# Optimization experiments

Measured on AMD Instinct MI355X. Metric: run time of the kernel, lower is better.

The kernel has to match this reference:

```python
import jax, jax.numpy as jnp
import numpy as np

EPS = 1e-5

def _bn_bcn(x, g, b):
    # BatchNorm1d on [B, C, N], training mode: stats over (B, N) per channel
    m = x.mean(axis=(0, 2), keepdims=True)
    v = x.var(axis=(0, 2), keepdims=True)
    return g[None, :, None] * (x - m) * jax.lax.rsqrt(v + EPS) + b[None, :, None]

def _bn_bc(x, g, b):
    # BatchNorm1d on [B, C]
    m = x.mean(axis=0)
    v = x.var(axis=0)
    return g * (x - m) * jax.lax.rsqrt(v + EPS) + b

def _symmetric_orthogonalization(x9):
    # x9: [B, 9] -> [B, 3, 3] in SO(3)
    m = x9.reshape(-1, 3, 3)
    u, s, vt = jnp.linalg.svd(m, full_matrices=False)
    det = jnp.linalg.det(jnp.matmul(u, vt))[:, None, None]
    vt = jnp.concatenate([vt[:, :2, :], vt[:, 2:, :] * det], axis=1)
    return jnp.matmul(u, vt)

def setup_inputs() -> dict:
    key = jax.random.key(0)
    ks = jax.random.split(key, 24)
    B, N = 32, 2048
    def lin(k, out_c, in_c):
        return jax.random.normal(k, (out_c, in_c), jnp.float32) / np.sqrt(in_c)
    inp = {}
    inp['x'] = jax.random.normal(ks[0], (B, 3, N), jnp.float32)
    # conv1x1 weights (kernel size 1 -> per-point linear)
    inp['w1'] = lin(ks[1], 64, 3);    inp['b1'] = jnp.zeros((64,), jnp.float32)
    inp['g1'] = jnp.ones((64,), jnp.float32);   inp['be1'] = jnp.zeros((64,), jnp.float32)
    inp['w2'] = lin(ks[2], 128, 64);  inp['b2'] = jnp.zeros((128,), jnp.float32)
    inp['g2'] = jnp.ones((128,), jnp.float32);  inp['be2'] = jnp.zeros((128,), jnp.float32)
    inp['w3'] = lin(ks[3], 1024, 128); inp['b3'] = jnp.zeros((1024,), jnp.float32)
    inp['g3'] = jnp.ones((1024,), jnp.float32); inp['be3'] = jnp.zeros((1024,), jnp.float32)
    inp['wf1'] = lin(ks[4], 512, 1024); inp['bf1'] = jnp.zeros((512,), jnp.float32)
    inp['gf1'] = jnp.ones((512,), jnp.float32); inp['bef1'] = jnp.zeros((512,), jnp.float32)
    inp['wf2'] = lin(ks[5], 256, 512);  inp['bf2'] = jnp.zeros((256,), jnp.float32)
    inp['gf2'] = jnp.ones((256,), jnp.float32); inp['bef2'] = jnp.zeros((256,), jnp.float32)
    inp['wp'] = lin(ks[6], 12, 256);    inp['bp'] = jnp.zeros((12,), jnp.float32)
    return inp

def reference(x, w1, b1, g1, be1, w2, b2, g2, be2, w3, b3, g3, be3,
              wf1, bf1, gf1, bef1, wf2, bf2, gf2, bef2, wp, bp):
    B = x.shape[0]
    h = jax.nn.relu(_bn_bcn(jnp.einsum('bdn,od->bon', x, w1) + b1[None, :, None], g1, be1))
    h = jax.nn.relu(_bn_bcn(jnp.einsum('bdn,od->bon', h, w2) + b2[None, :, None], g2, be2))
    h = _bn_bcn(jnp.einsum('bdn,od->bon', h, w3) + b3[None, :, None], g3, be3)
    h = jnp.max(h, axis=2)                      # global max pool -> [B, 1024]
    h = jax.nn.relu(_bn_bc(h @ wf1.T + bf1, gf1, bef1))
    h = jax.nn.relu(_bn_bc(h @ wf2.T + bf2, gf2, bef2))
    p = h @ wp.T + bp                           # [B, 12]
    R = _symmetric_orthogonalization(p[:, :9])  # [B, 3, 3]
    t = p[:, 9:].reshape(-1, 3, 1)
    top = jnp.concatenate([R, t], axis=2)       # [B, 3, 4]
    pad = jnp.broadcast_to(jnp.array([0.0, 0.0, 0.0, 1.0], dtype=x.dtype), (B, 1, 4))
    return jnp.concatenate([top, pad], axis=1)  # [B, 4, 4]
```

## Files before the change

kernel.cpp:

```cpp
#include <hip/hip_runtime.h>


#define NPT 2048
#define C1 64
#define C2 128
#define EPSV 1e-5f

typedef __attribute__((ext_vector_type(8))) _Float16 half8;
typedef __attribute__((ext_vector_type(4))) float floatx4;

#define OFF_Y1H   0
#define OFF_Y2H   2097152
#define OFF_Z     6291456
#define OFF_SUM1  (OFF_Z)
#define OFF_SQ1   (OFF_Z+64)
#define OFF_SUM2  (OFF_Z+128)
#define OFF_SQ2   (OFF_Z+256)
#define OFF_SUM3  (OFF_Z+384)
#define OFF_SQ3   (OFF_Z+1408)
#define OFF_F1R   (OFF_Z+2432)
#define OFF_F2R   (OFF_Z+18816)
#define ZN        27008
#define OFF_MX    (OFF_Z+27008)
#define OFF_MN    (OFF_MX+131072)
#define OFF_POOL  (OFF_MN+131072)
#define OFF_W3H   (OFF_POOL+32768)
#define OFF_W2H   (OFF_W3H+65536)
#define WS_FLOATS (OFF_W2H+4096)

static __device__ inline unsigned short f16r(float f) {
  _Float16 h = (_Float16)f;
  return __builtin_bit_cast(unsigned short, h);
}
static __device__ inline float h2f(unsigned short u) {
  return (float)__builtin_bit_cast(_Float16, u);
}
static __device__ inline int SW(int n, int cb) { return n ^ (((n >> 3) ^ cb) & 7); }

__global__ __launch_bounds__(256) void k_conv1(const float* __restrict__ x,
    const float* __restrict__ w1, const float* __restrict__ b1,
    unsigned short* __restrict__ y1h, float* __restrict__ sum1, float* __restrict__ sq1)
{
  int idx4 = blockIdx.x * 256 + threadIdx.x;
  int n4 = idx4 & 511;
  int o  = (idx4 >> 9) & 63;
  int b  = idx4 >> 15;
  const float4* xr = (const float4*)(x + (size_t)b * 3 * NPT);
  float4 x0 = xr[n4], x1 = xr[512 + n4], x2 = xr[1024 + n4];
  float wa = w1[o*3], wb = w1[o*3+1], wc = w1[o*3+2], bb = b1[o];
  float4 v;
  v.x = fmaf(wa, x0.x, fmaf(wb, x1.x, fmaf(wc, x2.x, bb)));
  v.y = fmaf(wa, x0.y, fmaf(wb, x1.y, fmaf(wc, x2.y, bb)));
  v.z = fmaf(wa, x0.z, fmaf(wb, x1.z, fmaf(wc, x2.z, bb)));
  v.w = fmaf(wa, x0.w, fmaf(wb, x1.w, fmaf(wc, x2.w, bb)));
  ushort4 p;
  p.x = f16r(v.x); p.y = f16r(v.y); p.z = f16r(v.z); p.w = f16r(v.w);
  ((ushort4*)y1h)[idx4] = p;
  float s = v.x + v.y + v.z + v.w;
  float q = v.x*v.x + v.y*v.y + v.z*v.z + v.w*v.w;
  for (int off = 32; off; off >>= 1) { s += __shfl_down(s, off); q += __shfl_down(q, off); }
  __shared__ float red[8];
  int lane = threadIdx.x & 63, wv = threadIdx.x >> 6;
  if (!lane) { red[wv] = s; red[4 + wv] = q; }
  __syncthreads();
  if (!threadIdx.x) {
    atomicAdd(&sum1[o], red[0] + red[1] + red[2] + red[3]);
    atomicAdd(&sq1[o],  red[4] + red[5] + red[6] + red[7]);
  }
}

__global__ __launch_bounds__(256) void k_cvt(const float* __restrict__ w3,
    const float* __restrict__ w2, unsigned short* __restrict__ w3h,
    unsigned short* __restrict__ w2h)
{
  int idx4 = blockIdx.x * 256 + threadIdx.x;
  const float4* src; ushort4* dst; int k;
  if (idx4 < 32768) { src = (const float4*)w3; dst = (ushort4*)w3h; k = idx4; }
  else               { src = (const float4*)w2; dst = (ushort4*)w2h; k = idx4 - 32768; }
  float4 v = src[k];
  ushort4 o;
  o.x = f16r(v.x); o.y = f16r(v.y); o.z = f16r(v.z); o.w = f16r(v.w);
  dst[k] = o;
}

__global__ __launch_bounds__(256, 2) void k_conv2(const unsigned short* __restrict__ y1h,
    const unsigned short* __restrict__ w2h, const float* __restrict__ b2,
    const float* __restrict__ sum1, const float* __restrict__ sq1,
    const float* __restrict__ g1, const float* __restrict__ be1,
    unsigned short* __restrict__ y2h, float* __restrict__ sum2, float* __restrict__ sq2)
{
  __shared__ unsigned short w2s[8 * 128 * 8];
  __shared__ unsigned short h1s[8 * 64 * 8];
  __shared__ float bn1[64][2];
  __shared__ float sred[2][128][2];
  int t = threadIdx.x;
  int bi = blockIdx.x;
  int b = bi >> 5, ns = bi & 31;
  int n0 = ns * 64;
  int w = t >> 6, lane = t & 63;
  int ow = w & 1, nw = w >> 1;
  int quad = lane >> 4, l15 = lane & 15;

  if (t < 64) {
    float m = sum1[t] * (1.f / 65536.f);
    float v = fmaf(-m, m, sq1[t] * (1.f / 65536.f));
    float ia = g1[t] * rsqrtf(v + EPSV);
    bn1[t][0] = ia; bn1[t][1] = fmaf(-ia, m, be1[t]);
  }
  for (int i = 0; i < 4; ++i) {
    int idx = i * 256 + t;
    int o = idx >> 3, cb = idx & 7;
    uint4 v = *(const uint4*)(w2h + o * 64 + cb * 8);
    int op = (o + cb) & 127;
    *(uint4*)&w2s[(cb * 128 + op) * 8] = v;
  }
  __syncthreads();

  half8 af[4][2];
  #pragma unroll
  for (int ti = 0; ti < 4; ++ti)
    #pragma unroll
    for (int s = 0; s < 2; ++s) {
      int cb = s * 4 + quad;
      int o = ow * 64 + ti * 16 + l15;
      int op = (o + cb) & 127;
      af[ti][s] = *(const half8*)&w2s[(cb * 128 + op) * 8];
    }
  float breg[4][4];
  #pragma unroll
  for (int ti = 0; ti < 4; ++ti)
    #pragma unroll
    for (int r = 0; r < 4; ++r)
      breg[ti][r] = b2[ow * 64 + ti * 16 + quad * 4 + r];

  {
    int cg = t >> 5, ng = t & 31;
    int c0 = cg * 8, nn = ng * 2;
    float av[8], sv[8];
    #pragma unroll
    for (int i = 0; i < 8; ++i) { av[i] = bn1[c0 + i][0]; sv[i] = bn1[c0 + i][1]; }
    const unsigned short* yb = y1h + (size_t)(b * C1 + c0) * NPT + n0 + nn;
    float v0[8], v1[8];
    #pragma unroll
    for (int i = 0; i < 8; ++i) {
      unsigned u = *(const unsigned*)(yb + (size_t)i * NPT);
      v0[i] = fmaxf(fmaf(av[i], h2f((unsigned short)(u & 0xffffu)), sv[i]), 0.f);
      v1[i] = fmaxf(fmaf(av[i], h2f((unsigned short)(u >> 16)), sv[i]), 0.f);
    }
    uint4 pk;
    pk.x = (unsigned)f16r(v0[0]) | ((unsigned)f16r(v0[1]) << 16);
    pk.y = (unsigned)f16r(v0[2]) | ((unsigned)f16r(v0[3]) << 16);
    pk.z = (unsigned)f16r(v0[4]) | ((unsigned)f16r(v0[5]) << 16);
    pk.w = (unsigned)f16r(v0[6]) | ((unsigned)f16r(v0[7]) << 16);
    *(uint4*)&h1s[(cg * 64 + SW(nn, cg)) * 8] = pk;
    pk.x = (unsigned)f16r(v1[0]) | ((unsigned)f16r(v1[1]) << 16);
    pk.y = (unsigned)f16r(v1[2]) | ((unsigned)f16r(v1[3]) << 16);
    pk.z = (unsigned)f16r(v1[4]) | ((unsigned)f16r(v1[5]) << 16);
    pk.w = (unsigned)f16r(v1[6]) | ((unsigned)f16r(v1[7]) << 16);
    *(uint4*)&h1s[(cg * 64 + SW(nn + 1, cg)) * 8] = pk;
  }
  __syncthreads();

  floatx4 acc[4][2];
  #pragma unroll
  for (int ti = 0; ti < 4; ++ti)
    #pragma unroll
    for (int nt = 0; nt < 2; ++nt) acc[ti][nt] = (floatx4){0.f, 0.f, 0.f, 0.f};
  #pragma unroll
  for (int s = 0; s < 2; ++s) {
    int cb = s * 4 + quad;
    half8 bf[2];
    #pragma unroll
    for (int nt = 0; nt < 2; ++nt) {
      int n = nw * 32 + nt * 16 + l15;
      bf[nt] = *(const half8*)&h1s[(cb * 64 + SW(n, cb)) * 8];
    }
    #pragma unroll
    for (int ti = 0; ti < 4; ++ti) {
      acc[ti][0] = __builtin_amdgcn_mfma_f32_16x16x32_f16(af[ti][s], bf[0], acc[ti][0], 0, 0, 0);
      acc[ti][1] = __builtin_amdgcn_mfma_f32_16x16x32_f16(af[ti][s], bf[1], acc[ti][1], 0, 0, 0);
    }
  }

  float sm[4][4], sq[4][4];
  #pragma unroll
  for (int ti = 0; ti < 4; ++ti)
    #pragma unroll
    for (int r = 0; r < 4; ++r) { sm[ti][r] = 0.f; sq[ti][r] = 0.f; }
  #pragma unroll
  for (int ti = 0; ti < 4; ++ti) {
    int o = ow * 64 + ti * 16 + quad * 4;
    #pragma unroll
    for (int nt = 0; nt < 2; ++nt) {
      int n = n0 + nw * 32 + nt * 16 + l15;
      #pragma unroll
      for (int r = 0; r < 4; ++r) {
        float val = acc[ti][nt][r] + breg[ti][r];
        y2h[(size_t)(b * C2 + o + r) * NPT + n] = f16r(val);
        sm[ti][r] += val;
        sq[ti][r] = fmaf(val, val, sq[ti][r]);
      }
    }
  }
  #pragma unroll
  for (int ti = 0; ti < 4; ++ti)
    #pragma unroll
    for (int r = 0; r < 4; ++r) {
      #pragma unroll
      for (int m = 1; m < 16; m <<= 1) {
        sm[ti][r] += __shfl_xor(sm[ti][r], m, 16);
        sq[ti][r] += __shfl_xor(sq[ti][r], m, 16);
      }
    }
  if (l15 == 0) {
    #pragma unroll
    for (int ti = 0; ti < 4; ++ti)
      #pragma unroll
      for (int r = 0; r < 4; ++r) {
        int oloc = ow * 64 + ti * 16 + quad * 4 + r;
        sred[nw][oloc][0] = sm[ti][r];
        sred[nw][oloc][1] = sq[ti][r];
      }
  }
  __syncthreads();
  if (t < 128) {
    atomicAdd(&sum2[t], sred[0][t][0] + sred[1][t][0]);
    atomicAdd(&sq2[t],  sred[0][t][1] + sred[1][t][1]);
  }
}

__global__ __launch_bounds__(256, 2) void k_conv3(const unsigned short* __restrict__ y2h,
    const unsigned short* __restrict__ w3h, const float* __restrict__ b3,
    const float* __restrict__ sum2, const float* __restrict__ sq2,
    const float* __restrict__ g2, const float* __restrict__ be2,
    float* __restrict__ mxb, float* __restrict__ mnb,
    float* __restrict__ sum3, float* __restrict__ sq3)
{
  __shared__ unsigned short w3s[16 * 128 * 8];
  __shared__ unsigned short h2s[16 * 64 * 8];
  __shared__ float sred[2][128][4];
  __shared__ float bn2[128][2];
  int t = threadIdx.x;
  int bi = blockIdx.x;
  int ot_blk = bi >> 7;
  int b  = (bi >> 2) & 31;
  int ns = bi & 3;
  int o0 = ot_blk * 128;
  int n_base = ns * 512;
  int w = t >> 6, lane = t & 63;
  int ow = w & 1, nw = w >> 1;
  int quad = lane >> 4, l15 = lane & 15;

  if (t < 128) {
    float m = sum2[t] * (1.f / 65536.f);
    float v = fmaf(-m, m, sq2[t] * (1.f / 65536.f));
    float ia = g2[t] * rsqrtf(v + EPSV);
    bn2[t][0] = ia; bn2[t][1] = fmaf(-ia, m, be2[t]);
  }
  for (int i = 0; i < 8; ++i) {
    int idx = i * 256 + t;
    int o = idx >> 4, cb = idx & 15;
    uint4 v = *(const uint4*)(w3h + (size_t)(o0 + o) * 128 + cb * 8);
    int op = (o + cb) & 127;
    *(uint4*)&w3s[(cb * 128 + op) * 8] = v;
  }
  __syncthreads();

  half8 af[4][4];
  #pragma unroll
  for (int ti = 0; ti < 4; ++ti)
    #pragma unroll
    for (int s = 0; s < 4; ++s) {
      int cb = s * 4 + quad;
      int o = ow * 64 + ti * 16 + l15;
      int op = (o + cb) & 127;
      af[ti][s] = *(const half8*)&w3s[(cb * 128 + op) * 8];
    }

  float breg[4][4], mx[4][4], mn[4][4], sm[4][4], sq[4][4];
  #pragma unroll
  for (int ti = 0; ti < 4; ++ti)
    #pragma unroll
    for (int r = 0; r < 4; ++r) {
      breg[ti][r] = b3[o0 + ow * 64 + ti * 16 + quad * 4 + r];
      mx[ti][r] = -3.4e38f; mn[ti][r] = 3.4e38f; sm[ti][r] = 0.f; sq[ti][r] = 0.f;
    }

  int cg = t >> 4, ng = t & 15;
  int c0 = cg * 8, nn = ng * 4;
  float av[8], sv[8];
  #pragma unroll
  for (int i = 0; i < 8; ++i) { av[i] = bn2[c0 + i][0]; sv[i] = bn2[c0 + i][1]; }

  for (int nc = 0; nc < 8; ++nc) {
    int n0 = n_base + nc * 64;
    __syncthreads();
    {
      float4 m[8];
      const unsigned short* yb = y2h + (size_t)(b * C2 + c0) * NPT + n0 + nn;
      #pragma unroll
      for (int i = 0; i < 8; ++i) {
        ushort4 u = *(const ushort4*)(yb + (size_t)i * NPT);
        m[i].x = fmaxf(fmaf(av[i], h2f(u.x), sv[i]), 0.f);
        m[i].y = fmaxf(fmaf(av[i], h2f(u.y), sv[i]), 0.f);
        m[i].z = fmaxf(fmaf(av[i], h2f(u.z), sv[i]), 0.f);
        m[i].w = fmaxf(fmaf(av[i], h2f(u.w), sv[i]), 0.f);
      }
      #define ST_J(j, comp) { \
        uint4 pk; \
        pk.x = (unsigned)f16r(m[0].comp) | ((unsigned)f16r(m[1].comp) << 16); \
        pk.y = (unsigned)f16r(m[2].comp) | ((unsigned)f16r(m[3].comp) << 16); \
        pk.z = (unsigned)f16r(m[4].comp) | ((unsigned)f16r(m[5].comp) << 16); \
        pk.w = (unsigned)f16r(m[6].comp) | ((unsigned)f16r(m[7].comp) << 16); \
        *(uint4*)&h2s[(cg * 64 + SW(nn + j, cg)) * 8] = pk; }
      ST_J(0, x) ST_J(1, y) ST_J(2, z) ST_J(3, w)
      #undef ST_J
    }
    __syncthreads();

    floatx4 acc[4][2];
    #pragma unroll
    for (int ti = 0; ti < 4; ++ti)
      #pragma unroll
      for (int nt = 0; nt < 2; ++nt) acc[ti][nt] = (floatx4){0.f, 0.f, 0.f, 0.f};
    #pragma unroll
    for (int s = 0; s < 4; ++s) {
      int cb = s * 4 + quad;
      half8 bf[2];
      #pragma unroll
      for (int nt = 0; nt < 2; ++nt) {
        int n = nw * 32 + nt * 16 + l15;
        bf[nt] = *(const half8*)&h2s[(cb * 64 + SW(n, cb)) * 8];
      }
      #pragma unroll
      for (int ti = 0; ti < 4; ++ti) {
        acc[ti][0] = __builtin_amdgcn_mfma_f32_16x16x32_f16(af[ti][s], bf[0], acc[ti][0], 0, 0, 0);
        acc[ti][1] = __builtin_amdgcn_mfma_f32_16x16x32_f16(af[ti][s], bf[1], acc[ti][1], 0, 0, 0);
      }
    }
    #pragma unroll
    for (int ti = 0; ti < 4; ++ti)
      #pragma unroll
      for (int nt = 0; nt < 2; ++nt)
        #pragma unroll
        for (int r = 0; r < 4; ++r) {
          float v = acc[ti][nt][r] + breg[ti][r];
          mx[ti][r] = fmaxf(mx[ti][r], v);
          mn[ti][r] = fminf(mn[ti][r], v);
          sm[ti][r] += v;
          sq[ti][r] = fmaf(v, v, sq[ti][r]);
        }
  }

  #pragma unroll
  for (int ti = 0; ti < 4; ++ti)
    #pragma unroll
    for (int r = 0; r < 4; ++r) {
      #pragma unroll
      for (int m = 1; m < 16; m <<= 1) {
        mx[ti][r] = fmaxf(mx[ti][r], __shfl_xor(mx[ti][r], m, 16));
        mn[ti][r] = fminf(mn[ti][r], __shfl_xor(mn[ti][r], m, 16));
        sm[ti][r] += __shfl_xor(sm[ti][r], m, 16);
        sq[ti][r] += __shfl_xor(sq[ti][r], m, 16);
      }
    }
  if (l15 == 0) {
    #pragma unroll
    for (int ti = 0; ti < 4; ++ti)
      #pragma unroll
      for (int r = 0; r < 4; ++r) {
        int oloc = ow * 64 + ti * 16 + quad * 4 + r;
        sred[nw][oloc][0] = mx[ti][r];
        sred[nw][oloc][1] = mn[ti][r];
        sred[nw][oloc][2] = sm[ti][r];
        sred[nw][oloc][3] = sq[ti][r];
      }
  }
  __syncthreads();
  if (t < 128) {
    int o = o0 + t;
    mxb[ns * 32768 + b * 1024 + o] = fmaxf(sred[0][t][0], sred[1][t][0]);
    mnb[ns * 32768 + b * 1024 + o] = fminf(sred[0][t][1], sred[1][t][1]);
    atomicAdd(&sum3[o], sred[0][t][2] + sred[1][t][2]);
    atomicAdd(&sq3[o],  sred[0][t][3] + sred[1][t][3]);
  }
}

__global__ __launch_bounds__(256) void k_pooled(const float* __restrict__ sum3,
    const float* __restrict__ sq3, const float* __restrict__ g3,
    const float* __restrict__ be3, const float* __restrict__ mxb,
    const float* __restrict__ mnb, float* __restrict__ pool)
{
  int idx4 = blockIdx.x * 256 + threadIdx.x;
  int c4 = idx4 & 255;
  float4 S = ((const float4*)sum3)[c4];
  float4 Q = ((const float4*)sq3)[c4];
  float4 G = ((const float4*)g3)[c4];
  float4 Be = ((const float4*)be3)[c4];
  float4 a, s;
  const float inv = 1.f / 65536.f;
  #define MK(c) { float m = S.c * inv; float v = fmaf(-m, m, Q.c * inv); \
                  a.c = G.c * rsqrtf(v + EPSV); s.c = fmaf(-a.c, m, Be.c); }
  MK(x) MK(y) MK(z) MK(w)
  #undef MK
  float4 mx = ((const float4*)mxb)[idx4];
  float4 mn = ((const float4*)mnb)[idx4];
  #pragma unroll
  for (int sl = 1; sl < 4; ++sl) {
    float4 mxs = ((const float4*)mxb)[idx4 + sl * 8192];
    float4 mns = ((const float4*)mnb)[idx4 + sl * 8192];
    mx.x = fmaxf(mx.x, mxs.x); mx.y = fmaxf(mx.y, mxs.y);
    mx.z = fmaxf(mx.z, mxs.z); mx.w = fmaxf(mx.w, mxs.w);
    mn.x = fminf(mn.x, mns.x); mn.y = fminf(mn.y, mns.y);
    mn.z = fminf(mn.z, mns.z); mn.w = fminf(mn.w, mns.w);
  }
  float4 r;
  r.x = fmaf(a.x, (a.x >= 0.f ? mx.x : mn.x), s.x);
  r.y = fmaf(a.y, (a.y >= 0.f ? mx.y : mn.y), s.y);
  r.z = fmaf(a.z, (a.z >= 0.f ? mx.z : mn.z), s.z);
  r.w = fmaf(a.w, (a.w >= 0.f ? mx.w : mn.w), s.w);
  ((float4*)pool)[idx4] = r;
}

__global__ __launch_bounds__(256) void k_fc1(const float* __restrict__ pool,
    const float* __restrict__ wf1, const float* __restrict__ bf1,
    float* __restrict__ f1r)
{
  __shared__ float ins[32 * 128];
  int t = threadIdx.x;
  int f0 = blockIdx.x * 32;
  int k0 = blockIdx.y * 128;
  #pragma unroll
  for (int i = 0; i < 4; ++i) {
    int idx = i * 256 + t;
    int b = idx >> 5, k4 = idx & 31;
    *(float4*)&ins[b * 128 + k4 * 4] = *(const float4*)(pool + (size_t)b * 1024 + k0 + k4 * 4);
  }
  __syncthreads();
  int f = t & 31, bq = t >> 5;
  int bl = bq * 4;
  const float4* wr = (const float4*)(wf1 + (size_t)(f0 + f) * 1024 + k0);
  float acc0 = 0.f, acc1 = 0.f, acc2 = 0.f, acc3 = 0.f;
  #pragma unroll
  for (int k4 = 0; k4 < 32; ++k4) {
    float4 wv = wr[k4];
    float4 i0 = *(const float4*)&ins[(bl + 0) * 128 + k4 * 4];
    float4 i1 = *(const float4*)&ins[(bl + 1) * 128 + k4 * 4];
    float4 i2 = *(const float4*)&ins[(bl + 2) * 128 + k4 * 4];
    float4 i3 = *(const float4*)&ins[(bl + 3) * 128 + k4 * 4];
    acc0 = fmaf(wv.x, i0.x, fmaf(wv.y, i0.y, fmaf(wv.z, i0.z, fmaf(wv.w, i0.w, acc0))));
    acc1 = fmaf(wv.x, i1.x, fmaf(wv.y, i1.y, fmaf(wv.z, i1.z, fmaf(wv.w, i1.w, acc1))));
    acc2 = fmaf(wv.x, i2.x, fmaf(wv.y, i2.y, fmaf(wv.z, i2.z, fmaf(wv.w, i2.w, acc2))));
    acc3 = fmaf(wv.x, i3.x, fmaf(wv.y, i3.y, fmaf(wv.z, i3.z, fmaf(wv.w, i3.w, acc3))));
  }
  float bs = (blockIdx.y == 0) ? bf1[f0 + f] : 0.f;
  atomicAdd(&f1r[(size_t)(bl + 0) * 512 + f0 + f], acc0 + bs);
  atomicAdd(&f1r[(size_t)(bl + 1) * 512 + f0 + f], acc1 + bs);
  atomicAdd(&f1r[(size_t)(bl + 2) * 512 + f0 + f], acc2 + bs);
  atomicAdd(&f1r[(size_t)(bl + 3) * 512 + f0 + f], acc3 + bs);
}

__global__ __launch_bounds__(256) void k_fc2(const float* __restrict__ f1r,
    const float* __restrict__ wf2, const float* __restrict__ bf2,
    const float* __restrict__ gf1, const float* __restrict__ bef1,
    float* __restrict__ f2r)
{
  __shared__ float ins[32 * 64];
  __shared__ float bnA[64], bnS[64];
  int t = threadIdx.x;
  int f0 = blockIdx.x * 32;
  int k0 = blockIdx.y * 64;
  #pragma unroll
  for (int i = 0; i < 2; ++i) {
    int idx = i * 256 + t;
    int b = idx >> 4, k4 = idx & 15;
    *(float4*)&ins[b * 64 + k4 * 4] = *(const float4*)(f1r + (size_t)b * 512 + k0 + k4 * 4);
  }
  __syncthreads();
  if (t < 64) {
    float s = 0.f, q = 0.f;
    #pragma unroll
    for (int b = 0; b < 32; ++b) {
      float x = ins[b * 64 + t];
      s += x; q = fmaf(x, x, q);
    }
    float m = s * (1.f / 32.f);
    float v = fmaf(-m, m, q * (1.f / 32.f));
    float a = gf1[k0 + t] * rsqrtf(v + EPSV);
    bnA[t] = a; bnS[t] = fmaf(-a, m, bef1[k0 + t]);
  }
  __syncthreads();
  #pragma unroll
  for (int i = 0; i < 2; ++i) {
    int idx = i * 256 + t;
    int b = idx >> 4, k4 = idx & 15;
    float4 v = *(const float4*)&ins[b * 64 + k4 * 4];
    v.x = fmaxf(fmaf(bnA[k4*4+0], v.x, bnS[k4*4+0]), 0.f);
    v.y = fmaxf(fmaf(bnA[k4*4+1], v.y, bnS[k4*4+1]), 0.f);
    v.z = fmaxf(fmaf(bnA[k4*4+2], v.z, bnS[k4*4+2]), 0.f);
    v.w = fmaxf(fmaf(bnA[k4*4+3], v.w, bnS[k4*4+3]), 0.f);
    *(float4*)&ins[b * 64 + k4 * 4] = v;
  }
  __syncthreads();
  int f = t & 31, bq = t >> 5;
  int bl = bq * 4;
  const float4* wr = (const float4*)(wf2 + (size_t)(f0 + f) * 512 + k0);
  float acc0 = 0.f, acc1 = 0.f, acc2 = 0.f, acc3 = 0.f;
  #pragma unroll
  for (int k4 = 0; k4 < 16; ++k4) {
    float4 wv = wr[k4];
    float4 i0 = *(const float4*)&ins[(bl + 0) * 64 + k4 * 4];
    float4 i1 = *(const float4*)&ins[(bl + 1) * 64 + k4 * 4];
    float4 i2 = *(const float4*)&ins[(bl + 2) * 64 + k4 * 4];
    float4 i3 = *(const float4*)&ins[(bl + 3) * 64 + k4 * 4];
    acc0 = fmaf(wv.x, i0.x, fmaf(wv.y, i0.y, fmaf(wv.z, i0.z, fmaf(wv.w, i0.w, acc0))));
    acc1 = fmaf(wv.x, i1.x, fmaf(wv.y, i1.y, fmaf(wv.z, i1.z, fmaf(wv.w, i1.w, acc1))));
    acc2 = fmaf(wv.x, i2.x, fmaf(wv.y, i2.y, fmaf(wv.z, i2.z, fmaf(wv.w, i2.w, acc2))));
    acc3 = fmaf(wv.x, i3.x, fmaf(wv.y, i3.y, fmaf(wv.z, i3.z, fmaf(wv.w, i3.w, acc3))));
  }
  float bs = (blockIdx.y == 0) ? bf2[f0 + f] : 0.f;
  atomicAdd(&f2r[(size_t)(bl + 0) * 256 + f0 + f], acc0 + bs);
  atomicAdd(&f2r[(size_t)(bl + 1) * 256 + f0 + f], acc1 + bs);
  atomicAdd(&f2r[(size_t)(bl + 2) * 256 + f0 + f], acc2 + bs);
  atomicAdd(&f2r[(size_t)(bl + 3) * 256 + f0 + f], acc3 + bs);
}

__global__ __launch_bounds__(384) void k_head(const float* __restrict__ f2r,
    const float* __restrict__ gf2, const float* __restrict__ bef2,
    const float* __restrict__ wp, const float* __restrict__ bp,
    float* __restrict__ out)
{
  __shared__ float pS[32 * 12];
  __shared__ float bnf[256][2];
  int t = threadIdx.x;
  if (t < 256) {
    float s = 0.f, q = 0.f;
    #pragma unroll
    for (int b = 0; b < 32; ++b) {
      float x = f2r[b * 256 + t];
      s += x; q = fmaf(x, x, q);
    }
    float m = s * (1.f / 32.f);
    float v = fmaf(-m, m, q * (1.f / 32.f));
    float a = gf2[t] * rsqrtf(v + EPSV);
    bnf[t][0] = a; bnf[t][1] = fmaf(-a, m, bef2[t]);
  }
  __syncthreads();
  {
    int b = t / 12, j = t % 12;
    const float* w = wp + j * 256;
    const float* fr = f2r + b * 256;
    float acc = bp[j];
    #pragma unroll 8
    for (int c = 0; c < 256; ++c) {
      float h = fmaxf(fmaf(bnf[c][0], fr[c], bnf[c][1]), 0.f);
      acc = fmaf(w[c], h, acc);
    }
    pS[t] = acc;
  }
  __syncthreads();
  if (t < 32) {
    const float* p = &pS[t * 12];
    float m00=p[0],m01=p[1],m02=p[2],m10=p[3],m11=p[4],m12=p[5],m20=p[6],m21=p[7],m22=p[8];
    float P[4][4];
    P[0][0]=m00+m11+m22; P[0][1]=m21-m12;     P[0][2]=m02-m20;     P[0][3]=m10-m01;
    P[1][1]=m00-m11-m22; P[1][2]=m01+m10;     P[1][3]=m02+m20;
    P[2][2]=m11-m00-m22; P[2][3]=m12+m21;
    P[3][3]=m22-m00-m11;
    P[1][0]=P[0][1]; P[2][0]=P[0][2]; P[3][0]=P[0][3];
    P[2][1]=P[1][2]; P[3][1]=P[1][3]; P[3][2]=P[2][3];
    float fn = sqrtf(m00*m00+m01*m01+m02*m02+m10*m10+m11*m11+m12*m12+m20*m20+m21*m21+m22*m22);
    float inv = 1.f / (2.f * fn + 1e-30f);
    #pragma unroll
    for (int i = 0; i < 4; ++i)
      #pragma unroll
      for (int j = 0; j < 4; ++j) P[i][j] *= inv;
    P[0][0] += 1.f; P[1][1] += 1.f; P[2][2] += 1.f; P[3][3] += 1.f;
    for (int it = 0; it < 16; ++it) {
      float Q[4][4];
      #pragma unroll
      for (int i = 0; i < 4; ++i)
        #pragma unroll
        for (int j = 0; j < 4; ++j)
          Q[i][j] = P[i][0]*P[0][j] + P[i][1]*P[1][j] + P[i][2]*P[2][j] + P[i][3]*P[3][j];
      float mxa = 0.f;
      #pragma unroll
      for (int i = 0; i < 4; ++i)
        #pragma unroll
        for (int j = 0; j < 4; ++j) mxa = fmaxf(mxa, fabsf(Q[i][j]));
      float r = 1.f / mxa;
      #pragma unroll
      for (int i = 0; i < 4; ++i)
        #pragma unroll
        for (int j = 0; j < 4; ++j) P[i][j] = Q[i][j] * r;
    }
    float bestn = -1.f; int bj = 0;
    #pragma unroll
    for (int j = 0; j < 4; ++j) {
      float nn = P[0][j]*P[0][j] + P[1][j]*P[1][j] + P[2][j]*P[2][j] + P[3][j]*P[3][j];
      if (nn > bestn) { bestn = nn; bj = j; }
    }
    float qw = P[0][bj], qx = P[1][bj], qy = P[2][bj], qz = P[3][bj];
    float qn = rsqrtf(qw*qw + qx*qx + qy*qy + qz*qz);
    qw *= qn; qx *= qn; qy *= qn; qz *= qn;
    float* ob = out + t * 16;
    ob[0]  = 1.f - 2.f*(qy*qy + qz*qz);
    ob[1]  = 2.f*(qx*qy - qw*qz);
    ob[2]  = 2.f*(qx*qz + qw*qy);
    ob[3]  = p[9];
    ob[4]  = 2.f*(qx*qy + qw*qz);
    ob[5]  = 1.f - 2.f*(qx*qx + qz*qz);
    ob[6]  = 2.f*(qy*qz - qw*qx);
    ob[7]  = p[10];
    ob[8]  = 2.f*(qx*qz - qw*qy);
    ob[9]  = 2.f*(qy*qz + qw*qx);
    ob[10] = 1.f - 2.f*(qx*qx + qy*qy);
    ob[11] = p[11];
    ob[12] = 0.f; ob[13] = 0.f; ob[14] = 0.f; ob[15] = 1.f;
  }
}

extern "C" void kernel_launch(void* const* d_in, const int* in_sizes, int n_in,
                              void* d_out, int out_size, void* d_ws, size_t ws_size,
                              hipStream_t stream)
{
  (void)in_sizes; (void)n_in; (void)out_size;
  if (ws_size < (size_t)WS_FLOATS * sizeof(float)) return;
  const float* x   = (const float*)d_in[0];
  const float* w1  = (const float*)d_in[1];
  const float* b1  = (const float*)d_in[2];
  const float* g1  = (const float*)d_in[3];
  const float* be1 = (const float*)d_in[4];
  const float* w2  = (const float*)d_in[5];
  const float* b2  = (const float*)d_in[6];
  const float* g2  = (const float*)d_in[7];
  const float* be2 = (const float*)d_in[8];
  const float* w3  = (const float*)d_in[9];
  const float* b3  = (const float*)d_in[10];
  const float* g3  = (const float*)d_in[11];
  const float* be3 = (const float*)d_in[12];
  const float* wf1 = (const float*)d_in[13];
  const float* bf1 = (const float*)d_in[14];
  const float* gf1 = (const float*)d_in[15];
  const float* bef1= (const float*)d_in[16];
  const float* wf2 = (const float*)d_in[17];
  const float* bf2 = (const float*)d_in[18];
  const float* gf2 = (const float*)d_in[19];
  const float* bef2= (const float*)d_in[20];
  const float* wp  = (const float*)d_in[21];
  const float* bp  = (const float*)d_in[22];
  float* ws  = (float*)d_ws;
  float* out = (float*)d_out;
  unsigned short* y1h = (unsigned short*)(ws + OFF_Y1H);
  unsigned short* y2h = (unsigned short*)(ws + OFF_Y2H);
  unsigned short* w3h = (unsigned short*)(ws + OFF_W3H);
  unsigned short* w2h = (unsigned short*)(ws + OFF_W2H);

  hipMemsetAsync((void*)(ws + OFF_Z), 0, ZN * sizeof(float), stream);
  k_cvt<<<136, 256, 0, stream>>>(w3, w2, w3h, w2h);
  k_conv1<<<4096, 256, 0, stream>>>(x, w1, b1, y1h, ws + OFF_SUM1, ws + OFF_SQ1);
  k_conv2<<<1024, 256, 0, stream>>>(y1h, w2h, b2, ws + OFF_SUM1, ws + OFF_SQ1, g1, be1,
                                    y2h, ws + OFF_SUM2, ws + OFF_SQ2);
  k_conv3<<<1024, 256, 0, stream>>>(y2h, w3h, b3, ws + OFF_SUM2, ws + OFF_SQ2, g2, be2,
                                    ws + OFF_MX, ws + OFF_MN, ws + OFF_SUM3, ws + OFF_SQ3);
  k_pooled<<<32, 256, 0, stream>>>(ws + OFF_SUM3, ws + OFF_SQ3, g3, be3,
                                   ws + OFF_MX, ws + OFF_MN, ws + OFF_POOL);
  k_fc1<<<dim3(16, 8), 256, 0, stream>>>(ws + OFF_POOL, wf1, bf1, ws + OFF_F1R);
  k_fc2<<<dim3(8, 8), 256, 0, stream>>>(ws + OFF_F1R, wf2, bf2, gf1, bef1, ws + OFF_F2R);
  k_head<<<1, 384, 0, stream>>>(ws + OFF_F2R, gf2, bef2, wp, bp, out);
}
```

Before: 254.4 us.

## Derive BN1 stats from input moments; pre-transpose activations into point-major layouts

Layer-1 BatchNorm statistics are now computed analytically from the 3x3 second moments of the input, collected in a new small reduction kernel, so conv1 no longer needs its atomic stat pass. conv1 then writes BN+ReLU-applied fp16 activations in point-major layout. A separate k_bnrelu2 kernel applies BN2+ReLU and transposes the result, which lets conv2 and conv3 stage tiles into shared memory with plain vector copies instead of per-tile normalization. conv3 runs half as many blocks, each covering a longer N range, and the pooled kernel merges two partial max/min slices instead of four. The FC unroll factors are also reduced. The cost is an extra kernel launch and an extra round trip through global memory for h2.

```diff
diff --git a/kernel.cpp b/kernel.cpp
--- a/kernel.cpp
+++ b/kernel.cpp
@@ -9,21 +9,21 @@
 typedef __attribute__((ext_vector_type(8))) _Float16 half8;
 typedef __attribute__((ext_vector_type(4))) float floatx4;
 
-#define OFF_Y1H   0
+#define OFF_H1T   0
 #define OFF_Y2H   2097152
-#define OFF_Z     6291456
-#define OFF_SUM1  (OFF_Z)
-#define OFF_SQ1   (OFF_Z+64)
-#define OFF_SUM2  (OFF_Z+128)
-#define OFF_SQ2   (OFF_Z+256)
-#define OFF_SUM3  (OFF_Z+384)
-#define OFF_SQ3   (OFF_Z+1408)
-#define OFF_F1R   (OFF_Z+2432)
-#define OFF_F2R   (OFF_Z+18816)
-#define ZN        27008
-#define OFF_MX    (OFF_Z+27008)
-#define OFF_MN    (OFF_MX+131072)
-#define OFF_POOL  (OFF_MN+131072)
+#define OFF_H2T   6291456
+#define OFF_Z     10485760
+#define OFF_XS    (OFF_Z)
+#define OFF_SUM2  (OFF_Z+16)
+#define OFF_SQ2   (OFF_Z+144)
+#define OFF_SUM3  (OFF_Z+272)
+#define OFF_SQ3   (OFF_Z+1296)
+#define OFF_F1R   (OFF_Z+2320)
+#define OFF_F2R   (OFF_Z+18704)
+#define ZN        26896
+#define OFF_MX    (OFF_Z+26896)
+#define OFF_MN    (OFF_MX+65536)
+#define OFF_POOL  (OFF_MN+65536)
 #define OFF_W3H   (OFF_POOL+32768)
 #define OFF_W2H   (OFF_W3H+65536)
 #define WS_FLOATS (OFF_W2H+4096)
@@ -37,36 +37,35 @@
 }
 static __device__ inline int SW(int n, int cb) { return n ^ (((n >> 3) ^ cb) & 7); }
 
-__global__ __launch_bounds__(256) void k_conv1(const float* __restrict__ x,
-    const float* __restrict__ w1, const float* __restrict__ b1,
-    unsigned short* __restrict__ y1h, float* __restrict__ sum1, float* __restrict__ sq1)
+__global__ __launch_bounds__(256) void k_xstat(const float* __restrict__ x,
+                                               float* __restrict__ xs)
 {
   int idx4 = blockIdx.x * 256 + threadIdx.x;
-  int n4 = idx4 & 511;
-  int o  = (idx4 >> 9) & 63;
-  int b  = idx4 >> 15;
+  int n4 = idx4 & 511, b = idx4 >> 9;
   const float4* xr = (const float4*)(x + (size_t)b * 3 * NPT);
   float4 x0 = xr[n4], x1 = xr[512 + n4], x2 = xr[1024 + n4];
-  float wa = w1[o*3], wb = w1[o*3+1], wc = w1[o*3+2], bb = b1[o];
-  float4 v;
-  v.x = fmaf(wa, x0.x, fmaf(wb, x1.x, fmaf(wc, x2.x, bb)));
-  v.y = fmaf(wa, x0.y, fmaf(wb, x1.y, fmaf(wc, x2.y, bb)));
-  v.z = fmaf(wa, x0.z, fmaf(wb, x1.z, fmaf(wc, x2.z, bb)));
-  v.w = fmaf(wa, x0.w, fmaf(wb, x1.w, fmaf(wc, x2.w, bb)));
-  ushort4 p;
-  p.x = f16r(v.x); p.y = f16r(v.y); p.z = f16r(v.z); p.w = f16r(v.w);
-  ((ushort4*)y1h)[idx4] = p;
-  float s = v.x + v.y + v.z + v.w;
-  float q = v.x*v.x + v.y*v.y + v.z*v.z + v.w*v.w;
-  for (int off = 32; off; off >>= 1) { s += __shfl_down(s, off); q += __shfl_down(q, off); }
-  __shared__ float red[8];
+  float v[9];
+  v[0] = x0.x + x0.y + x0.z + x0.w;
+  v[1] = x1.x + x1.y + x1.z + x1.w;
+  v[2] = x2.x + x2.y + x2.z + x2.w;
+  v[3] = x0.x*x0.x + x0.y*x0.y + x0.z*x0.z + x0.w*x0.w;
+  v[4] = x1.x*x1.x + x1.y*x1.y + x1.z*x1.z + x1.w*x1.w;
+  v[5] = x2.x*x2.x + x2.y*x2.y + x2.z*x2.z + x2.w*x2.w;
+  v[6] = x0.x*x1.x + x0.y*x1.y + x0.z*x1.z + x0.w*x1.w;
+  v[7] = x0.x*x2.x + x0.y*x2.y + x0.z*x2.z + x0.w*x2.w;
+  v[8] = x1.x*x2.x + x1.y*x2.y + x1.z*x2.z + x1.w*x2.w;
+  #pragma unroll
+  for (int k = 0; k < 9; ++k)
+    for (int off = 32; off; off >>= 1) v[k] += __shfl_down(v[k], off);
+  __shared__ float red[4][9];
   int lane = threadIdx.x & 63, wv = threadIdx.x >> 6;
-  if (!lane) { red[wv] = s; red[4 + wv] = q; }
-  __syncthreads();
-  if (!threadIdx.x) {
-    atomicAdd(&sum1[o], red[0] + red[1] + red[2] + red[3]);
-    atomicAdd(&sq1[o],  red[4] + red[5] + red[6] + red[7]);
-  }
+  if (!lane)
+    #pragma unroll
+    for (int k = 0; k < 9; ++k) red[wv][k] = v[k];
+  __syncthreads();
+  if (threadIdx.x < 9)
+    atomicAdd(&xs[threadIdx.x], red[0][threadIdx.x] + red[1][threadIdx.x] +
+                                red[2][threadIdx.x] + red[3][threadIdx.x]);
 }
 
 __global__ __launch_bounds__(256) void k_cvt(const float* __restrict__ w3,
@@ -83,15 +82,54 @@
   dst[k] = o;
 }
 
-__global__ __launch_bounds__(256, 2) void k_conv2(const unsigned short* __restrict__ y1h,
+__global__ __launch_bounds__(256) void k_conv1(const float* __restrict__ x,
+    const float* __restrict__ w1, const float* __restrict__ b1,
+    const float* __restrict__ g1, const float* __restrict__ be1,
+    const float* __restrict__ xs, unsigned short* __restrict__ h1t)
+{
+  __shared__ float wc[64][4];
+  int t = threadIdx.x;
+  int bi = blockIdx.x;
+  int b = bi >> 3, nt = bi & 7;
+  if (t < 64) {
+    float w0 = w1[t*3], w1_ = w1[t*3+1], w2_ = w1[t*3+2], bb = b1[t];
+    const float invN = 1.f / 65536.f;
+    float wsx = (w0*xs[0] + w1_*xs[1] + w2_*xs[2]) * invN;
+    float mean = wsx + bb;
+    float Ey2 = (w0*w0*xs[3] + w1_*w1_*xs[4] + w2_*w2_*xs[5]
+               + 2.f*(w0*w1_*xs[6] + w0*w2_*xs[7] + w1_*w2_*xs[8])) * invN
+               + 2.f*bb*wsx + bb*bb;
+    float var = Ey2 - mean*mean;
+    float a = g1[t] * rsqrtf(var + EPSV);
+    wc[t][0] = a*w0; wc[t][1] = a*w1_; wc[t][2] = a*w2_;
+    wc[t][3] = be1[t] + a*(bb - mean);
+  }
+  __syncthreads();
+  int n = nt * 256 + t;
+  const float* xb = x + (size_t)b * 3 * NPT + n;
+  float x0 = xb[0], x1 = xb[NPT], x2 = xb[2*NPT];
+  unsigned short* orow = h1t + ((size_t)b * NPT + n) * C1;
+  #pragma unroll
+  for (int i = 0; i < 8; ++i) {
+    uint4 pk;
+    unsigned* pd = (unsigned*)&pk;
+    #pragma unroll
+    for (int j = 0; j < 4; ++j) {
+      int o = i*8 + j*2;
+      float h0 = fmaxf(fmaf(wc[o][0], x0, fmaf(wc[o][1], x1, fmaf(wc[o][2], x2, wc[o][3]))), 0.f);
+      float h1 = fmaxf(fmaf(wc[o+1][0], x0, fmaf(wc[o+1][1], x1, fmaf(wc[o+1][2], x2, wc[o+1][3]))), 0.f);
+      pd[j] = (unsigned)f16r(h0) | ((unsigned)f16r(h1) << 16);
+    }
+    *(uint4*)(orow + i * 8) = pk;
+  }
+}
+
+__global__ __launch_bounds__(256, 2) void k_conv2(const unsigned short* __restrict__ h1t,
     const unsigned short* __restrict__ w2h, const float* __restrict__ b2,
-    const float* __restrict__ sum1, const float* __restrict__ sq1,
-    const float* __restrict__ g1, const float* __restrict__ be1,
     unsigned short* __restrict__ y2h, float* __restrict__ sum2, float* __restrict__ sq2)
 {
   __shared__ unsigned short w2s[8 * 128 * 8];
   __shared__ unsigned short h1s[8 * 64 * 8];
-  __shared__ float bn1[64][2];
   __shared__ float sred[2][128][2];
   int t = threadIdx.x;
   int bi = blockIdx.x;
@@ -101,12 +139,6 @@
   int ow = w & 1, nw = w >> 1;
   int quad = lane >> 4, l15 = lane & 15;
 
-  if (t < 64) {
-    float m = sum1[t] * (1.f / 65536.f);
-    float v = fmaf(-m, m, sq1[t] * (1.f / 65536.f));
-    float ia = g1[t] * rsqrtf(v + EPSV);
-    bn1[t][0] = ia; bn1[t][1] = fmaf(-ia, m, be1[t]);
-  }
   for (int i = 0; i < 4; ++i) {
     int idx = i * 256 + t;
     int o = idx >> 3, cb = idx & 7;
@@ -114,6 +146,14 @@
     int op = (o + cb) & 127;
     *(uint4*)&w2s[(cb * 128 + op) * 8] = v;
   }
+  {
+    int n = t & 63, cp = t >> 6;
+    const unsigned short* src = h1t + ((size_t)b * NPT + n0 + n) * C1 + cp * 16;
+    uint4 v0 = *(const uint4*)(src);
+    uint4 v1 = *(const uint4*)(src + 8);
+    *(uint4*)&h1s[((2*cp)   * 64 + SW(n, 2*cp))   * 8] = v0;
+    *(uint4*)&h1s[((2*cp+1) * 64 + SW(n, 2*cp+1)) * 8] = v1;
+  }
   __syncthreads();
 
   half8 af[4][2];
@@ -132,34 +172,6 @@
     #pragma unroll
     for (int r = 0; r < 4; ++r)
       breg[ti][r] = b2[ow * 64 + ti * 16 + quad * 4 + r];
-
-  {
-    int cg = t >> 5, ng = t & 31;
-    int c0 = cg * 8, nn = ng * 2;
-    float av[8], sv[8];
-    #pragma unroll
-    for (int i = 0; i < 8; ++i) { av[i] = bn1[c0 + i][0]; sv[i] = bn1[c0 + i][1]; }
-    const unsigned short* yb = y1h + (size_t)(b * C1 + c0) * NPT + n0 + nn;
-    float v0[8], v1[8];
-    #pragma unroll
-    for (int i = 0; i < 8; ++i) {
-      unsigned u = *(const unsigned*)(yb + (size_t)i * NPT);
-      v0[i] = fmaxf(fmaf(av[i], h2f((unsigned short)(u & 0xffffu)), sv[i]), 0.f);
-      v1[i] = fmaxf(fmaf(av[i], h2f((unsigned short)(u >> 16)), sv[i]), 0.f);
-    }
-    uint4 pk;
-    pk.x = (unsigned)f16r(v0[0]) | ((unsigned)f16r(v0[1]) << 16);
-    pk.y = (unsigned)f16r(v0[2]) | ((unsigned)f16r(v0[3]) << 16);
-    pk.z = (unsigned)f16r(v0[4]) | ((unsigned)f16r(v0[5]) << 16);
-    pk.w = (unsigned)f16r(v0[6]) | ((unsigned)f16r(v0[7]) << 16);
-    *(uint4*)&h1s[(cg * 64 + SW(nn, cg)) * 8] = pk;
-    pk.x = (unsigned)f16r(v1[0]) | ((unsigned)f16r(v1[1]) << 16);
-    pk.y = (unsigned)f16r(v1[2]) | ((unsigned)f16r(v1[3]) << 16);
-    pk.z = (unsigned)f16r(v1[4]) | ((unsigned)f16r(v1[5]) << 16);
-    pk.w = (unsigned)f16r(v1[6]) | ((unsigned)f16r(v1[7]) << 16);
-    *(uint4*)&h1s[(cg * 64 + SW(nn + 1, cg)) * 8] = pk;
-  }
-  __syncthreads();
 
   floatx4 acc[4][2];
   #pragma unroll
@@ -229,34 +241,65 @@
   }
 }
 
-__global__ __launch_bounds__(256, 2) void k_conv3(const unsigned short* __restrict__ y2h,
-    const unsigned short* __restrict__ w3h, const float* __restrict__ b3,
+__global__ __launch_bounds__(256) void k_bnrelu2(const unsigned short* __restrict__ y2h,
     const float* __restrict__ sum2, const float* __restrict__ sq2,
     const float* __restrict__ g2, const float* __restrict__ be2,
+    unsigned short* __restrict__ h2t)
+{
+  __shared__ float bn[128][2];
+  int t = threadIdx.x;
+  int bi = blockIdx.x;
+  int b = bi >> 5, nt = bi & 31;
+  int n0 = nt * 64;
+  if (t < 128) {
+    float m = sum2[t] * (1.f / 65536.f);
+    float v = fmaf(-m, m, sq2[t] * (1.f / 65536.f));
+    float a = g2[t] * rsqrtf(v + EPSV);
+    bn[t][0] = a; bn[t][1] = fmaf(-a, m, be2[t]);
+  }
+  __syncthreads();
+  int coct = t & 15, ng = t >> 4;
+  int c0 = coct * 8, n = n0 + ng * 4;
+  float h[8][4];
+  #pragma unroll
+  for (int i = 0; i < 8; ++i) {
+    ushort4 u = *(const ushort4*)(y2h + (size_t)(b * C2 + c0 + i) * NPT + n);
+    float a = bn[c0 + i][0], s = bn[c0 + i][1];
+    h[i][0] = fmaxf(fmaf(a, h2f(u.x), s), 0.f);
+    h[i][1] = fmaxf(fmaf(a, h2f(u.y), s), 0.f);
+    h[i][2] = fmaxf(fmaf(a, h2f(u.z), s), 0.f);
+    h[i][3] = fmaxf(fmaf(a, h2f(u.w), s), 0.f);
+  }
+  #pragma unroll
+  for (int j = 0; j < 4; ++j) {
+    uint4 pk;
+    pk.x = (unsigned)f16r(h[0][j]) | ((unsigned)f16r(h[1][j]) << 16);
+    pk.y = (unsigned)f16r(h[2][j]) | ((unsigned)f16r(h[3][j]) << 16);
+    pk.z = (unsigned)f16r(h[4][j]) | ((unsigned)f16r(h[5][j]) << 16);
+    pk.w = (unsigned)f16r(h[6][j]) | ((unsigned)f16r(h[7][j]) << 16);
+    *(uint4*)(h2t + ((size_t)b * NPT + n + j) * C2 + c0) = pk;
+  }
+}
+
+__global__ __launch_bounds__(256, 2) void k_conv3(const unsigned short* __restrict__ h2t,
+    const unsigned short* __restrict__ w3h, const float* __restrict__ b3,
     float* __restrict__ mxb, float* __restrict__ mnb,
     float* __restrict__ sum3, float* __restrict__ sq3)
 {
   __shared__ unsigned short w3s[16 * 128 * 8];
   __shared__ unsigned short h2s[16 * 64 * 8];
   __shared__ float sred[2][128][4];
-  __shared__ float bn2[128][2];
   int t = threadIdx.x;
   int bi = blockIdx.x;
-  int ot_blk = bi >> 7;
-  int b  = (bi >> 2) & 31;
-  int ns = bi & 3;
+  int ot_blk = bi >> 6;
+  int b  = (bi >> 1) & 31;
+  int ns = bi & 1;
   int o0 = ot_blk * 128;
-  int n_base = ns * 512;
+  int n_base = ns * 1024;
   int w = t >> 6, lane = t & 63;
   int ow = w & 1, nw = w >> 1;
   int quad = lane >> 4, l15 = lane & 15;
 
-  if (t < 128) {
-    float m = sum2[t] * (1.f / 65536.f);
-    float v = fmaf(-m, m, sq2[t] * (1.f / 65536.f));
-    float ia = g2[t] * rsqrtf(v + EPSV);
-    bn2[t][0] = ia; bn2[t][1] = fmaf(-ia, m, be2[t]);
-  }
   for (int i = 0; i < 8; ++i) {
     int idx = i * 256 + t;
     int o = idx >> 4, cb = idx & 15;
@@ -286,35 +329,21 @@
       mx[ti][r] = -3.4e38f; mn[ti][r] = 3.4e38f; sm[ti][r] = 0.f; sq[ti][r] = 0.f;
     }
 
-  int cg = t >> 4, ng = t & 15;
-  int c0 = cg * 8, nn = ng * 4;
-  float av[8], sv[8];
-  #pragma unroll
-  for (int i = 0; i < 8; ++i) { av[i] = bn2[c0 + i][0]; sv[i] = bn2[c0 + i][1]; }
-
-  for (int nc = 0; nc < 8; ++nc) {
+  int sn = t & 63, cq = t >> 6;
+  for (int nc = 0; nc < 16; ++nc) {
     int n0 = n_base + nc * 64;
     __syncthreads();
     {
-      float4 m[8];
-      const unsigned short* yb = y2h + (size_t)(b * C2 + c0) * NPT + n0 + nn;
-      #pragma unroll
-      for (int i = 0; i < 8; ++i) {
-        ushort4 u = *(const ushort4*)(yb + (size_t)i * NPT);
-        m[i].x = fmaxf(fmaf(av[i], h2f(u.x), sv[i]), 0.f);
-        m[i].y = fmaxf(fmaf(av[i], h2f(u.y), sv[i]), 0.f);
-        m[i].z = fmaxf(fmaf(av[i], h2f(u.z), sv[i]), 0.f);
-        m[i].w = fmaxf(fmaf(av[i], h2f(u.w), sv[i]), 0.f);
-      }
-      #define ST_J(j, comp) { \
-        uint4 pk; \
-        pk.x = (unsigned)f16r(m[0].comp) | ((unsigned)f16r(m[1].comp) << 16); \
-        pk.y = (unsigned)f16r(m[2].comp) | ((unsigned)f16r(m[3].comp) << 16); \
-        pk.z = (unsigned)f16r(m[4].comp) | ((unsigned)f16r(m[5].comp) << 16); \
-        pk.w = (unsigned)f16r(m[6].comp) | ((unsigned)f16r(m[7].comp) << 16); \
-        *(uint4*)&h2s[(cg * 64 + SW(nn + j, cg)) * 8] = pk; }
-      ST_J(0, x) ST_J(1, y) ST_J(2, z) ST_J(3, w)
-      #undef ST_J
+      const unsigned short* src = h2t + ((size_t)b * NPT + n0 + sn) * C2 + cq * 32;
+      uint4 v0 = *(const uint4*)(src);
+      uint4 v1 = *(const uint4*)(src + 8);
+      uint4 v2 = *(const uint4*)(src + 16);
+      uint4 v3 = *(const uint4*)(src + 24);
+      int cb0 = cq * 4;
+      *(uint4*)&h2s[((cb0 + 0) * 64 + SW(sn, cb0 + 0)) * 8] = v0;
+      *(uint4*)&h2s[((cb0 + 1) * 64 + SW(sn, cb0 + 1)) * 8] = v1;
+      *(uint4*)&h2s[((cb0 + 2) * 64 + SW(sn, cb0 + 2)) * 8] = v2;
+      *(uint4*)&h2s[((cb0 + 3) * 64 + SW(sn, cb0 + 3)) * 8] = v3;
     }
     __syncthreads();
 
@@ -405,10 +434,9 @@
   #undef MK
   float4 mx = ((const float4*)mxb)[idx4];
   float4 mn = ((const float4*)mnb)[idx4];
-  #pragma unroll
-  for (int sl = 1; sl < 4; ++sl) {
-    float4 mxs = ((const float4*)mxb)[idx4 + sl * 8192];
-    float4 mns = ((const float4*)mnb)[idx4 + sl * 8192];
+  {
+    float4 mxs = ((const float4*)mxb)[idx4 + 8192];
+    float4 mns = ((const float4*)mnb)[idx4 + 8192];
     mx.x = fmaxf(mx.x, mxs.x); mx.y = fmaxf(mx.y, mxs.y);
     mx.z = fmaxf(mx.z, mxs.z); mx.w = fmaxf(mx.w, mxs.w);
     mn.x = fminf(mn.x, mns.x); mn.y = fminf(mn.y, mns.y);
@@ -441,7 +469,7 @@
   int bl = bq * 4;
   const float4* wr = (const float4*)(wf1 + (size_t)(f0 + f) * 1024 + k0);
   float acc0 = 0.f, acc1 = 0.f, acc2 = 0.f, acc3 = 0.f;
-  #pragma unroll
+  #pragma unroll 4
   for (int k4 = 0; k4 < 32; ++k4) {
     float4 wv = wr[k4];
     float4 i0 = *(const float4*)&ins[(bl + 0) * 128 + k4 * 4];
@@ -506,7 +534,7 @@
   int bl = bq * 4;
   const float4* wr = (const float4*)(wf2 + (size_t)(f0 + f) * 512 + k0);
   float acc0 = 0.f, acc1 = 0.f, acc2 = 0.f, acc3 = 0.f;
-  #pragma unroll
+  #pragma unroll 4
   for (int k4 = 0; k4 < 16; ++k4) {
     float4 wv = wr[k4];
     float4 i0 = *(const float4*)&ins[(bl + 0) * 64 + k4 * 4];
@@ -516,7 +544,7 @@
     acc0 = fmaf(wv.x, i0.x, fmaf(wv.y, i0.y, fmaf(wv.z, i0.z, fmaf(wv.w, i0.w, acc0))));
     acc1 = fmaf(wv.x, i1.x, fmaf(wv.y, i1.y, fmaf(wv.z, i1.z, fmaf(wv.w, i1.w, acc1))));
     acc2 = fmaf(wv.x, i2.x, fmaf(wv.y, i2.y, fmaf(wv.z, i2.z, fmaf(wv.w, i2.w, acc2))));
-    acc3 = fmaf(wv.x, i3.x, fmaf(wv.y, i3.y, fmaf(wv.z, i3.z, fmaf(wv.w, i3.w, acc3))));
+    acc3 = fmaf(wv.x, i3.x, fmaf(wv.y, i3.y, fmaf(wv.w, i3.w, fmaf(wv.z, i3.z, acc3))));
   }
   float bs = (blockIdx.y == 0) ? bf2[f0 + f] : 0.f;
   atomicAdd(&f2r[(size_t)(bl + 0) * 256 + f0 + f], acc0 + bs);
@@ -651,18 +679,20 @@
   const float* bp  = (const float*)d_in[22];
   float* ws  = (float*)d_ws;
   float* out = (float*)d_out;
-  unsigned short* y1h = (unsigned short*)(ws + OFF_Y1H);
+  unsigned short* h1t = (unsigned short*)(ws + OFF_H1T);
   unsigned short* y2h = (unsigned short*)(ws + OFF_Y2H);
+  unsigned short* h2t = (unsigned short*)(ws + OFF_H2T);
   unsigned short* w3h = (unsigned short*)(ws + OFF_W3H);
   unsigned short* w2h = (unsigned short*)(ws + OFF_W2H);
 
   hipMemsetAsync((void*)(ws + OFF_Z), 0, ZN * sizeof(float), stream);
   k_cvt<<<136, 256, 0, stream>>>(w3, w2, w3h, w2h);
-  k_conv1<<<4096, 256, 0, stream>>>(x, w1, b1, y1h, ws + OFF_SUM1, ws + OFF_SQ1);
-  k_conv2<<<1024, 256, 0, stream>>>(y1h, w2h, b2, ws + OFF_SUM1, ws + OFF_SQ1, g1, be1,
-                                    y2h, ws + OFF_SUM2, ws + OFF_SQ2);
-  k_conv3<<<1024, 256, 0, stream>>>(y2h, w3h, b3, ws + OFF_SUM2, ws + OFF_SQ2, g2, be2,
-                                    ws + OFF_MX, ws + OFF_MN, ws + OFF_SUM3, ws + OFF_SQ3);
+  k_xstat<<<64, 256, 0, stream>>>(x, ws + OFF_XS);
+  k_conv1<<<256, 256, 0, stream>>>(x, w1, b1, g1, be1, ws + OFF_XS, h1t);
+  k_conv2<<<1024, 256, 0, stream>>>(h1t, w2h, b2, y2h, ws + OFF_SUM2, ws + OFF_SQ2);
+  k_bnrelu2<<<1024, 256, 0, stream>>>(y2h, ws + OFF_SUM2, ws + OFF_SQ2, g2, be2, h2t);
+  k_conv3<<<512, 256, 0, stream>>>(h2t, w3h, b3, ws + OFF_MX, ws + OFF_MN,
+                                   ws + OFF_SUM3, ws + OFF_SQ3);
   k_pooled<<<32, 256, 0, stream>>>(ws + OFF_SUM3, ws + OFF_SQ3, g3, be3,
                                    ws + OFF_MX, ws + OFF_MN, ws + OFF_POOL);
   k_fc1<<<dim3(16, 8), 256, 0, stream>>>(ws + OFF_POOL, wf1, bf1, ws + OFF_F1R);
```

Result: faster. 221.4 us (-13.0%).
